# Optimization experiments

Measured on AMD Instinct MI355X. Metric: run time of the kernel, lower is better.

## Reference

```python
import jax, jax.numpy as jnp
import numpy as np

N1 = 512
N2 = 512
N = N1 + N2
NEG_SLOPE = 0.2


def _build_edges(n1, n2):
    # inside: fully connected within each set, both directions
    s1, d1 = np.triu_indices(n1, 1)
    s2, d2 = np.triu_indices(n2, 1)
    is_ = np.concatenate([s1, s2 + n1])
    id_ = np.concatenate([d1, d2 + n1])
    inside = np.stack([np.concatenate([is_, id_]), np.concatenate([id_, is_])])
    # cross: fully connected bipartite, both directions
    cs = np.repeat(np.arange(n1), n2)
    cd = np.tile(np.arange(n1, n1 + n2), n1)
    cross = np.stack([np.concatenate([cs, cd]), np.concatenate([cd, cs])])
    # PyG GATConv default add_self_loops=True
    loops = np.arange(n1 + n2)
    self_e = np.stack([loops, loops])
    inside = np.concatenate([inside, self_e], axis=1)
    cross = np.concatenate([cross, self_e], axis=1)
    return inside.astype(np.int32), cross.astype(np.int32)


def setup_inputs() -> dict:
    key = jax.random.key(0)
    ks = jax.random.split(key, 12)
    inside_edge, cross_edge = _build_edges(N1, N2)
    s = 0.1
    return {
        'desc1': jax.random.normal(ks[0], (N1, 128), jnp.float32),
        'desc2': jax.random.normal(ks[1], (N2, 128), jnp.float32),
        'W1': jax.random.normal(ks[2], (128, 128), jnp.float32) * s,
        'a_src1': jax.random.normal(ks[3], (128, 1), jnp.float32) * s,
        'a_dst1': jax.random.normal(ks[4], (128, 1), jnp.float32) * s,
        'b1': jnp.zeros((128,), jnp.float32),
        'W2': jax.random.normal(ks[5], (128, 128), jnp.float32) * s,
        'a_src2': jax.random.normal(ks[6], (1, 128), jnp.float32) * s,
        'a_dst2': jax.random.normal(ks[7], (1, 128), jnp.float32) * s,
        'b2': jnp.zeros((128,), jnp.float32),
        'inside_edge': jnp.asarray(inside_edge),
        'cross_edge': jnp.asarray(cross_edge),
    }


def gat_conv(x, edge_index, W, a_src, a_dst, bias, heads, out_ch, concat):
    # x: [N, F_in]; edge_index: [2, E] (self-loops already included)
    n = x.shape[0]
    src, dst = edge_index[0], edge_index[1]
    h = (x @ W).reshape(n, heads, out_ch)                 # [N, H, C]
    a_s = jnp.sum(h * a_src, axis=-1)                     # [N, H]
    a_d = jnp.sum(h * a_dst, axis=-1)                     # [N, H]
    e = jax.nn.leaky_relu(a_s[src] + a_d[dst], NEG_SLOPE)  # [E, H]
    # segment (scatter) softmax over incoming edges of each dst node
    m = jax.ops.segment_max(e, dst, num_segments=n)
    ex = jnp.exp(e - m[dst])
    denom = jax.ops.segment_sum(ex, dst, num_segments=n)
    alpha = ex / (denom[dst] + 1e-16)                     # [E, H]
    out = jax.ops.segment_sum(alpha[:, :, None] * h[src], dst, num_segments=n)  # [N, H, C]
    out = out.reshape(n, heads * out_ch) if concat else out.mean(axis=1)
    return out + bias


def reference(desc1, desc2, W1, a_src1, a_dst1, b1, W2, a_src2, a_dst2, b2, inside_edge, cross_edge):
    x = jnp.concatenate([desc1, desc2], axis=0)  # [N, 128]
    for _ in range(2):
        x = jax.nn.elu(gat_conv(x, inside_edge, W1, a_src1, a_dst1, b1, 128, 1, True))
        x = jax.nn.elu(gat_conv(x, cross_edge, W1, a_src1, a_dst1, b1, 128, 1, True))
    x = gat_conv(x, cross_edge, W2, a_src2, a_dst2, b2, 1, 128, False)  # [N, 128]
    return x
```

## Files before the change

kernel.cpp:

```cpp
#include <hip/hip_runtime.h>
#include <hip/hip_bf16.h>


typedef __hip_bfloat16 bf16;

__device__ __forceinline__ float b2f(bf16 x) { return __bfloat162float(x); }

__device__ __forceinline__ int detect_bf16(const void* desc1) {
  const unsigned* u = (const unsigned*)desc1;
  int hits = 0;
#pragma unroll 8
  for (int i = 0; i < 256; ++i) {
    unsigned e = (u[i] >> 7) & 0xFFu;
    hits += (e >= 100u && e <= 140u) ? 1 : 0;
  }
  return hits >= 200 ? 1 : 0;
}

__device__ __forceinline__ float load_in(const void* p, int i, int bf) {
  return bf ? b2f(((const bf16*)p)[i]) : ((const float*)p)[i];
}

__global__ __launch_bounds__(256) void prep_kernel(
    const void* __restrict__ desc1, const void* __restrict__ desc2,
    const void* __restrict__ W1,   const void* __restrict__ as1,
    const void* __restrict__ ad1,  const void* __restrict__ b1,
    const void* __restrict__ W2,   const void* __restrict__ as2,
    const void* __restrict__ ad2,  const void* __restrict__ b2,
    float* __restrict__ xt, float* __restrict__ W1t, float* __restrict__ W2f,
    float* __restrict__ vecs, int* __restrict__ flag) {
  const int bf = detect_bf16(desc1);
  if (blockIdx.x == 0 && threadIdx.x == 0) *flag = bf;
  const int total = 131072 + 16384 + 16384 + 6 * 128;
  for (int idx = blockIdx.x * blockDim.x + threadIdx.x; idx < total;
       idx += gridDim.x * blockDim.x) {
    if (idx < 131072) {
      int c = idx & 127, n = idx >> 7;
      float v = (n < 512) ? load_in(desc1, idx, bf)
                          : load_in(desc2, idx - 65536, bf);
      xt[((c >> 2) * 1024 + n) * 4 + (c & 3)] = v;
    } else if (idx < 147456) {
      int i = idx - 131072;
      int k = i >> 7, hdd = i & 127;
      W1t[hdd * 128 + k] = load_in(W1, i, bf);
    } else if (idx < 163840) {
      W2f[idx - 147456] = load_in(W2, idx - 147456, bf);
    } else {
      int i = idx - 163840, o = i & 127;
      float v;
      if      (i < 128) v = load_in(as1, o, bf);
      else if (i < 256) v = load_in(ad1, o, bf);
      else if (i < 384) v = load_in(b1, o, bf);
      else if (i < 512) v = load_in(as2, o, bf);
      else if (i < 640) v = load_in(ad2, o, bf);
      else              v = load_in(b2, o, bf);
      vecs[i] = v;
    }
  }
}

__global__ __launch_bounds__(256, 2) void gemm_kernel(
    const float* __restrict__ xt_in, const float* __restrict__ W1t,
    float* __restrict__ Ht) {
  __shared__ float wcol[128];
  const int tid = threadIdx.x;
  const int hd = blockIdx.x & 127;
  const int chunk = blockIdx.x >> 7;
  const int node = chunk * 256 + tid;
  if (tid < 32) ((float4*)wcol)[tid] = ((const float4*)(W1t + hd * 128))[tid];
  __syncthreads();
  const float4* x4 = (const float4*)xt_in;
  float acc0 = 0.f, acc1 = 0.f;
  for (int cc = 0; cc < 32; cc += 8) {
    float4 xs[8];
#pragma unroll
    for (int u = 0; u < 8; ++u) xs[u] = x4[(cc + u) * 1024 + node];
#pragma unroll
    for (int u = 0; u < 8; ++u) {
      const int k = (cc + u) * 4;
      acc0 = fmaf(xs[u].x, wcol[k],     acc0);
      acc1 = fmaf(xs[u].y, wcol[k + 1], acc1);
      acc0 = fmaf(xs[u].z, wcol[k + 2], acc0);
      acc1 = fmaf(xs[u].w, wcol[k + 3], acc1);
    }
  }
  Ht[hd * 1024 + node] = acc0 + acc1;
}

template <int CROSS>
__global__ __launch_bounds__(256, 2) void attn_kernel(
    const float* __restrict__ Ht, float* __restrict__ xt_out,
    const float* __restrict__ vecs) {
  __shared__ __align__(16) float4 sE[512];
  const int tid  = threadIdx.x;
  const int hd   = blockIdx.x & 127;
  const int S    = (blockIdx.x >> 7) & 1;
  const int half = blockIdx.x >> 8;
  const int D    = CROSS ? (1 - S) : S;
  const float a_src = vecs[hd], a_dst = vecs[128 + hd], bias = vecs[256 + hd];
  const float* HtH = Ht + hd * 1024;

#pragma unroll
  for (int u = 0; u < 2; ++u) {
    const int i = u * 256 + tid;
    const float h = HtH[S * 512 + i];
    const float s = h * a_src;
    const float e1 = __expf(s), e2 = __expf(0.2f * s);
    sE[i] = make_float4(e1, e2, e1 * h, e2 * h);
  }
  const int j = half * 256 + tid;
  const float hD    = HtH[D * 512 + j];
  const float d_own = hD * a_dst;
  const float F1  = __expf(d_own), F2 = __expf(0.2f * d_own);
  const float eTh = __expf(-d_own);
  __syncthreads();

  float M1 = 0.f, M1h = 0.f, N2 = 0.f, N2h = 0.f;
#pragma unroll 8
  for (int i = 0; i < 512; ++i) {
    const float4 r = sE[i];
    const float m = (r.x >= eTh) ? 1.0f : 0.0f;
    const float n = (r.x >= eTh) ? 0.0f : 1.0f;
    M1  = fmaf(m, r.x, M1);
    M1h = fmaf(m, r.z, M1h);
    N2  = fmaf(n, r.y, N2);
    N2h = fmaf(n, r.w, N2h);
  }
  float den = fmaf(F1, M1,  F2 * N2);
  float num = fmaf(F1, M1h, F2 * N2h);
  if (CROSS) {
    const float t = hD * a_src + d_own;
    const float p = __expf(fmaxf(t, 0.2f * t));
    den += p;
    num = fmaf(p, hD, num);
  }
  float o = num / (den + 1e-16f) + bias;
  o = (o > 0.f) ? o : expm1f(o);
  xt_out[(((hd >> 2) * 1024) + D * 512 + j) * 4 + (hd & 3)] = o;
}

__global__ __launch_bounds__(256, 2) void mm2_kernel(
    const float* __restrict__ xt_in, const float* __restrict__ W2f,
    const float* __restrict__ vecs, float* __restrict__ h2,
    float* __restrict__ s2, float* __restrict__ d2) {
  __shared__ float rs[256], rd[256];
  const int tid = threadIdx.x;
  const int row = blockIdx.x * 2 + (tid >> 7);
  const int c = tid & 127;
  float acc0 = 0.f, acc1 = 0.f;
  {
    const float4* x4 = (const float4*)xt_in;
    for (int cc = 0; cc < 32; cc += 8) {
      float4 xb[8];
#pragma unroll
      for (int u = 0; u < 8; ++u) xb[u] = x4[(cc + u) * 1024 + row];
#pragma unroll
      for (int u = 0; u < 8; ++u) {
        const int k = (cc + u) * 4;
        acc0 = fmaf(xb[u].x, W2f[k * 128 + c],       acc0);
        acc1 = fmaf(xb[u].y, W2f[(k + 1) * 128 + c], acc1);
        acc0 = fmaf(xb[u].z, W2f[(k + 2) * 128 + c], acc0);
        acc1 = fmaf(xb[u].w, W2f[(k + 3) * 128 + c], acc1);
      }
    }
  }
  float acc = acc0 + acc1;
  h2[row * 128 + c] = acc;
  rs[tid] = acc * vecs[384 + c];
  rd[tid] = acc * vecs[512 + c];
  __syncthreads();
  for (int off = 64; off > 0; off >>= 1) {
    if ((tid & 127) < off) { rs[tid] += rs[tid + off]; rd[tid] += rd[tid + off]; }
    __syncthreads();
  }
  if ((tid & 127) == 0) {
    s2[row] = rs[tid];
    d2[row] = rd[tid];
  }
}

__global__ __launch_bounds__(256, 2) void att2_kernel(
    const float* __restrict__ h2, const float* __restrict__ s2,
    const float* __restrict__ d2, const float* __restrict__ vecs,
    void* __restrict__ out, const int* __restrict__ flag) {
  __shared__ __align__(16) float pT[512 * 2];
  const int tid = threadIdx.x;
  const int dstBase = blockIdx.x * 2;
  const int srcBase = (dstBase < 512) ? 512 : 0;

  for (int e = tid; e < 1024; e += 256) {
    int j = e >> 1, ld = e & 1;
    float t = s2[srcBase + j] + d2[dstBase + ld];
    pT[e] = __expf(fmaxf(t, 0.2f * t));
  }
  __syncthreads();

  const int c = tid & 127;
  const int g = tid >> 7;
  const int i0 = dstBase + g;
  float den = 0.f, num = 0.f;
  const float* hrow = h2 + srcBase * 128 + c;
  for (int j0 = 0; j0 < 512; j0 += 8) {
    float hb[8];
#pragma unroll
    for (int u = 0; u < 8; ++u) hb[u] = hrow[(j0 + u) * 128];
#pragma unroll
    for (int u = 0; u < 8; ++u) {
      float p = pT[(j0 + u) * 2 + g];
      den += p;
      num = fmaf(p, hb[u], num);
    }
  }
  float ts = s2[i0] + d2[i0];
  float ps = __expf(fmaxf(ts, 0.2f * ts));
  den += ps;
  num = fmaf(ps, h2[i0 * 128 + c], num);

  float o = num / (den + 1e-16f) + vecs[640 + c];
  if (*flag) ((bf16*)out)[i0 * 128 + c] = __float2bfloat16(o);
  else       ((float*)out)[i0 * 128 + c] = o;
}

extern "C" void kernel_launch(void* const* d_in, const int* in_sizes, int n_in,
                              void* d_out, int out_size, void* d_ws, size_t ws_size,
                              hipStream_t stream) {
  (void)in_sizes; (void)n_in; (void)out_size; (void)ws_size;
  float* ws   = (float*)d_ws;
  float* xtA  = ws;
  float* xtB  = ws + 131072;
  float* h2   = ws + 262144;
  float* Ht   = h2;
  float* W1t  = ws + 393216;
  float* W2f  = ws + 409600;
  float* vecs = ws + 425984;
  float* s2   = ws + 426752;
  float* d2   = ws + 427776;
  int*   flag = (int*)(ws + 428800);

  prep_kernel<<<256, 256, 0, stream>>>(d_in[0], d_in[1], d_in[2], d_in[3],
                                       d_in[4], d_in[5], d_in[6], d_in[7],
                                       d_in[8], d_in[9], xtA, W1t, W2f, vecs,
                                       flag);
  gemm_kernel<<<512, 256, 0, stream>>>(xtA, W1t, Ht);
  attn_kernel<0><<<512, 256, 0, stream>>>(Ht, xtB, vecs);
  gemm_kernel<<<512, 256, 0, stream>>>(xtB, W1t, Ht);
  attn_kernel<1><<<512, 256, 0, stream>>>(Ht, xtA, vecs);
  gemm_kernel<<<512, 256, 0, stream>>>(xtA, W1t, Ht);
  attn_kernel<0><<<512, 256, 0, stream>>>(Ht, xtB, vecs);
  gemm_kernel<<<512, 256, 0, stream>>>(xtB, W1t, Ht);
  attn_kernel<1><<<512, 256, 0, stream>>>(Ht, xtA, vecs);
  mm2_kernel<<<512, 256, 0, stream>>>(xtA, W2f, vecs, h2, s2, d2);
  att2_kernel<<<512, 256, 0, stream>>>(h2, s2, d2, vecs, d_out, flag);
}
```

Measured before the change: 196.5 us.

## Split attention destinations across lane groups and switch activations to plain transposed layout

The attention kernel now assigns each destination node to 8 lanes that each scan a strided eighth of the 512 sources, then combine partial sums with xor shuffles. This lets the launch grow from 512 to 4096 blocks, with a higher occupancy hint, to fix the low parallelism of the long serial source loop. In exchange, every block recomputes the shared source exponential table, so that setup work is repeated eight times more often. The activation buffer also moves from a float4-interleaved layout to a plain [channel][node] layout, and the GEMM kernels now use scalar loads instead of float4 loads.

```diff
diff --git a/kernel.cpp b/kernel.cpp
--- a/kernel.cpp
+++ b/kernel.cpp
@@ -38,7 +38,7 @@
       int c = idx & 127, n = idx >> 7;
       float v = (n < 512) ? load_in(desc1, idx, bf)
                           : load_in(desc2, idx - 65536, bf);
-      xt[((c >> 2) * 1024 + n) * 4 + (c & 3)] = v;
+      xt[c * 1024 + n] = v;
     } else if (idx < 147456) {
       int i = idx - 131072;
       int k = i >> 7, hdd = i & 127;
@@ -69,36 +69,33 @@
   const int node = chunk * 256 + tid;
   if (tid < 32) ((float4*)wcol)[tid] = ((const float4*)(W1t + hd * 128))[tid];
   __syncthreads();
-  const float4* x4 = (const float4*)xt_in;
   float acc0 = 0.f, acc1 = 0.f;
-  for (int cc = 0; cc < 32; cc += 8) {
-    float4 xs[8];
-#pragma unroll
-    for (int u = 0; u < 8; ++u) xs[u] = x4[(cc + u) * 1024 + node];
-#pragma unroll
-    for (int u = 0; u < 8; ++u) {
-      const int k = (cc + u) * 4;
-      acc0 = fmaf(xs[u].x, wcol[k],     acc0);
-      acc1 = fmaf(xs[u].y, wcol[k + 1], acc1);
-      acc0 = fmaf(xs[u].z, wcol[k + 2], acc0);
-      acc1 = fmaf(xs[u].w, wcol[k + 3], acc1);
+  for (int k0 = 0; k0 < 128; k0 += 8) {
+    float xb[8];
+#pragma unroll
+    for (int u = 0; u < 8; ++u) xb[u] = xt_in[(k0 + u) * 1024 + node];
+#pragma unroll
+    for (int u = 0; u < 8; u += 2) {
+      acc0 = fmaf(xb[u],     wcol[k0 + u],     acc0);
+      acc1 = fmaf(xb[u + 1], wcol[k0 + u + 1], acc1);
     }
   }
   Ht[hd * 1024 + node] = acc0 + acc1;
 }
 
 template <int CROSS>
-__global__ __launch_bounds__(256, 2) void attn_kernel(
+__global__ __launch_bounds__(256, 8) void attn_kernel(
     const float* __restrict__ Ht, float* __restrict__ xt_out,
     const float* __restrict__ vecs) {
   __shared__ __align__(16) float4 sE[512];
-  const int tid  = threadIdx.x;
-  const int hd   = blockIdx.x & 127;
-  const int S    = (blockIdx.x >> 7) & 1;
-  const int half = blockIdx.x >> 8;
-  const int D    = CROSS ? (1 - S) : S;
+  const int tid = threadIdx.x;
+  const int hd  = blockIdx.x & 127;
+  const int grp = blockIdx.x >> 7;
+  const int dj  = grp * 32 + (tid >> 3);
+  const int Sd  = dj >> 9;
+  const int S   = CROSS ? (1 - Sd) : Sd;
   const float a_src = vecs[hd], a_dst = vecs[128 + hd], bias = vecs[256 + hd];
-  const float* HtH = Ht + hd * 1024;
+  const float* __restrict__ HtH = Ht + hd * 1024;
 
 #pragma unroll
   for (int u = 0; u < 2; ++u) {
@@ -108,17 +105,17 @@
     const float e1 = __expf(s), e2 = __expf(0.2f * s);
     sE[i] = make_float4(e1, e2, e1 * h, e2 * h);
   }
-  const int j = half * 256 + tid;
-  const float hD    = HtH[D * 512 + j];
+  const float hD    = HtH[dj];
   const float d_own = hD * a_dst;
   const float F1  = __expf(d_own), F2 = __expf(0.2f * d_own);
   const float eTh = __expf(-d_own);
   __syncthreads();
 
+  const int l = tid & 7;
   float M1 = 0.f, M1h = 0.f, N2 = 0.f, N2h = 0.f;
-#pragma unroll 8
-  for (int i = 0; i < 512; ++i) {
-    const float4 r = sE[i];
+#pragma unroll 4
+  for (int ii = 0; ii < 64; ++ii) {
+    const float4 r = sE[ii * 8 + l];
     const float m = (r.x >= eTh) ? 1.0f : 0.0f;
     const float n = (r.x >= eTh) ? 0.0f : 1.0f;
     M1  = fmaf(m, r.x, M1);
@@ -126,17 +123,26 @@
     N2  = fmaf(n, r.y, N2);
     N2h = fmaf(n, r.w, N2h);
   }
-  float den = fmaf(F1, M1,  F2 * N2);
-  float num = fmaf(F1, M1h, F2 * N2h);
-  if (CROSS) {
-    const float t = hD * a_src + d_own;
-    const float p = __expf(fmaxf(t, 0.2f * t));
-    den += p;
-    num = fmaf(p, hD, num);
-  }
-  float o = num / (den + 1e-16f) + bias;
-  o = (o > 0.f) ? o : expm1f(o);
-  xt_out[(((hd >> 2) * 1024) + D * 512 + j) * 4 + (hd & 3)] = o;
+#pragma unroll
+  for (int off = 1; off < 8; off <<= 1) {
+    M1  += __shfl_xor(M1,  off);
+    M1h += __shfl_xor(M1h, off);
+    N2  += __shfl_xor(N2,  off);
+    N2h += __shfl_xor(N2h, off);
+  }
+  if (l == 0) {
+    float den = fmaf(F1, M1,  F2 * N2);
+    float num = fmaf(F1, M1h, F2 * N2h);
+    if (CROSS) {
+      const float t = hD * a_src + d_own;
+      const float p = __expf(fmaxf(t, 0.2f * t));
+      den += p;
+      num = fmaf(p, hD, num);
+    }
+    float o = num / (den + 1e-16f) + bias;
+    o = (o > 0.f) ? o : expm1f(o);
+    xt_out[hd * 1024 + dj] = o;
+  }
 }
 
 __global__ __launch_bounds__(256, 2) void mm2_kernel(
@@ -148,20 +154,14 @@
   const int row = blockIdx.x * 2 + (tid >> 7);
   const int c = tid & 127;
   float acc0 = 0.f, acc1 = 0.f;
-  {
-    const float4* x4 = (const float4*)xt_in;
-    for (int cc = 0; cc < 32; cc += 8) {
-      float4 xb[8];
-#pragma unroll
-      for (int u = 0; u < 8; ++u) xb[u] = x4[(cc + u) * 1024 + row];
-#pragma unroll
-      for (int u = 0; u < 8; ++u) {
-        const int k = (cc + u) * 4;
-        acc0 = fmaf(xb[u].x, W2f[k * 128 + c],       acc0);
-        acc1 = fmaf(xb[u].y, W2f[(k + 1) * 128 + c], acc1);
-        acc0 = fmaf(xb[u].z, W2f[(k + 2) * 128 + c], acc0);
-        acc1 = fmaf(xb[u].w, W2f[(k + 3) * 128 + c], acc1);
-      }
+  for (int k0 = 0; k0 < 128; k0 += 8) {
+    float xb[8];
+#pragma unroll
+    for (int u = 0; u < 8; ++u) xb[u] = xt_in[(k0 + u) * 1024 + row];
+#pragma unroll
+    for (int u = 0; u < 8; u += 2) {
+      acc0 = fmaf(xb[u],     W2f[(k0 + u) * 128 + c],     acc0);
+      acc1 = fmaf(xb[u + 1], W2f[(k0 + u + 1) * 128 + c], acc1);
     }
   }
   float acc = acc0 + acc1;
@@ -242,13 +242,13 @@
                                        d_in[8], d_in[9], xtA, W1t, W2f, vecs,
                                        flag);
   gemm_kernel<<<512, 256, 0, stream>>>(xtA, W1t, Ht);
-  attn_kernel<0><<<512, 256, 0, stream>>>(Ht, xtB, vecs);
+  attn_kernel<0><<<4096, 256, 0, stream>>>(Ht, xtB, vecs);
   gemm_kernel<<<512, 256, 0, stream>>>(xtB, W1t, Ht);
-  attn_kernel<1><<<512, 256, 0, stream>>>(Ht, xtA, vecs);
+  attn_kernel<1><<<4096, 256, 0, stream>>>(Ht, xtA, vecs);
   gemm_kernel<<<512, 256, 0, stream>>>(xtA, W1t, Ht);
-  attn_kernel<0><<<512, 256, 0, stream>>>(Ht, xtB, vecs);
+  attn_kernel<0><<<4096, 256, 0, stream>>>(Ht, xtB, vecs);
   gemm_kernel<<<512, 256, 0, stream>>>(xtB, W1t, Ht);
-  attn_kernel<1><<<512, 256, 0, stream>>>(Ht, xtA, vecs);
+  attn_kernel<1><<<4096, 256, 0, stream>>>(Ht, xtA, vecs);
   mm2_kernel<<<512, 256, 0, stream>>>(xtA, W2f, vecs, h2, s2, d2);
   att2_kernel<<<512, 256, 0, stream>>>(h2, s2, d2, vecs, d_out, flag);
 }
```

After: 195.6 us. No clear change (-0.4%).
